# Performance work log

Measured on AMD Instinct MI355X. Metric: run time of the kernel, lower is better.

The kernel has to match this reference:

```python
import jax, jax.numpy as jnp
import numpy as np

T, K = 2048, 6          # tokens, activated experts per token
DIM = 2048              # model dim
INTER = 1408            # moe intermediate dim
E = 16                  # routed experts (group_size, shared not fused)


def setup_inputs() -> dict:
    key = jax.random.key(0)
    k1, k2, k3, k4, k5, k6 = jax.random.split(key, 6)
    x = jax.random.normal(k1, (T, DIM), dtype=jnp.float32)
    weights = jax.random.uniform(k2, (T, K), dtype=jnp.float32)
    indices = jax.random.randint(k3, (T, K), 0, E, dtype=jnp.int64)
    s = 1.0 / np.sqrt(DIM)
    Wg = jax.random.normal(k4, (E, INTER, DIM), dtype=jnp.float32) * s
    Wu = jax.random.normal(k5, (E, INTER, DIM), dtype=jnp.float32) * s
    Wd = jax.random.normal(k6, (E, DIM, INTER), dtype=jnp.float32) * (1.0 / np.sqrt(INTER))
    return {"x": x, "weights": weights, "indices": indices,
            "Wg": Wg, "Wu": Wu, "Wd": Wd}


def reference(x, weights, indices, Wg, Wu, Wd):
    # per-token combine weight for each expert: [T, E]
    # gate_w[t, e] = sum_k weights[t, k] * (indices[t, k] == e)
    one_hot = jax.nn.one_hot(indices, E, dtype=x.dtype)        # [T, K, E]
    gate_w = jnp.einsum('tk,tke->te', weights, one_hot)        # [T, E]

    # SwiGLU expert FFN, dense over experts, combine folded pre-down-proj
    g = jnp.einsum('td,eid->tei', x, Wg)                       # [T, E, INTER]
    u = jnp.einsum('td,eid->tei', x, Wu)                       # [T, E, INTER]
    act = jax.nn.silu(g) * u                                   # [T, E, INTER]
    # y[t] = sum_e gate_w[t,e] * (act[t,e] @ Wd[e].T)
    y = jnp.einsum('tei,edi->td', act * gate_w[:, :, None], Wd)  # [T, DIM]
    return y
```

## Files before the change

kernel.cpp:

```cpp
#include <hip/hip_runtime.h>
#include <hip/hip_bf16.h>
#include <cstdint>

#define TT     2048
#define KSEL   6
#define DMODEL 2048
#define DINTER 1408
#define NE     16
#define PMAX   (TT * KSEL)

typedef short bf16x8 __attribute__((ext_vector_type(8)));
typedef float f32x4 __attribute__((ext_vector_type(4)));
typedef unsigned short u16;
typedef u16 u16x8 __attribute__((ext_vector_type(8)));

__device__ __forceinline__ u16 f2bf(float f) {
  union { float f; unsigned u; } v; v.f = f;
  return (u16)((v.u + 0x7FFFu + ((v.u >> 16) & 1u)) >> 16);
}

__device__ __forceinline__ void gl2lds16(const void* g, void* l) {
  __builtin_amdgcn_global_load_lds((const __attribute__((address_space(1))) void*)g,
                                   (__attribute__((address_space(3))) void*)l,
                                   16, 0, 0);
}

__global__ void k_gate(const float* __restrict__ w, const int* __restrict__ idx,
                       float* __restrict__ gate_w, int* __restrict__ counts) {
  int g = blockIdx.x * 256 + threadIdx.x;
  int t = g >> 4, e = g & 15;
  const int* ip = idx + t * KSEL;
  const float* wp = w + t * KSEL;
  float s = 0.f;
#pragma unroll
  for (int k = 0; k < KSEL; ++k) s += (ip[k] == e) ? wp[k] : 0.f;
  gate_w[g] = s;
  if (s != 0.f) atomicAdd(counts + e, 1);
}

__global__ void k_scan(const int* __restrict__ counts, int* __restrict__ offs) {
  if (threadIdx.x == 0 && blockIdx.x == 0) {
    int r = 0;
#pragma unroll
    for (int e = 0; e < NE; ++e) { offs[e] = r; r += counts[e]; }
    offs[NE] = r;
  }
}

__global__ void k_fill(const float* __restrict__ gate_w, const int* __restrict__ offs,
                       int* __restrict__ cursor, int* __restrict__ slot_tok,
                       float* __restrict__ slot_gate) {
  int g = blockIdx.x * 256 + threadIdx.x;
  int t = g >> 4, e = g & 15;
  float s = gate_w[g];
  if (s != 0.f) {
    int p = atomicAdd(cursor + e, 1);
    int sl = offs[e] + p;
    slot_tok[sl] = t;
    slot_gate[sl] = s;
  }
}

#define XV8   (TT * DMODEL / 8)
#define WV8   (NE * DINTER * DMODEL / 8)
__global__ void k_castall(const float* __restrict__ x,  u16* __restrict__ xb,
                          const float* __restrict__ wg, u16* __restrict__ wgb,
                          const float* __restrict__ wu, u16* __restrict__ wub,
                          const float* __restrict__ wd, u16* __restrict__ wdb) {
  const int total = XV8 + 3 * WV8;
  int stride = gridDim.x * 256;
  for (int i = blockIdx.x * 256 + threadIdx.x; i < total; i += stride) {
    const float* src; u16* dst; int j;
    if (i < XV8)                { src = x;  dst = xb;  j = i; }
    else if (i < XV8 + WV8)     { src = wg; dst = wgb; j = i - XV8; }
    else if (i < XV8 + 2 * WV8) { src = wu; dst = wub; j = i - XV8 - WV8; }
    else                        { src = wd; dst = wdb; j = i - XV8 - 2 * WV8; }
    const float4* p = (const float4*)src + (size_t)j * 2;
    float4 v0 = p[0], v1 = p[1];
    u16x8 o;
    o[0] = f2bf(v0.x); o[1] = f2bf(v0.y); o[2] = f2bf(v0.z); o[3] = f2bf(v0.w);
    o[4] = f2bf(v1.x); o[5] = f2bf(v1.y); o[6] = f2bf(v1.z); o[7] = f2bf(v1.w);
    *(u16x8*)(dst + (size_t)j * 8) = o;
  }
}


__global__ __launch_bounds__(256, 2) void k_gemm1(
    const u16* __restrict__ xb, const u16* __restrict__ wgb, const u16* __restrict__ wub,
    const int* __restrict__ slot_tok, const float* __restrict__ slot_gate,
    const int* __restrict__ offs, const int* __restrict__ counts,
    u16* __restrict__ act) {
  int b = blockIdx.x;
  int w = (b & 7) * 352 + (b >> 3);
  int mt = w & 15, rest = w >> 4;
  int it = rest % 11, e = rest / 11;

  int mcount = counts[e];
  if (mt * 128 >= mcount) return;
  int mrem = mcount - mt * 128; if (mrem > 128) mrem = 128;
  int slotBase = offs[e] + mt * 128;
  int iBase = it * 128;

  __shared__ u16 sA[128 * 64];
  __shared__ u16 sG[128 * 64];
  __shared__ u16 sU[128 * 64];
  __shared__ int tokLds[128];
  __shared__ float gateLds[128];

  int tid = threadIdx.x;
  if (tid < 128) {
    int rl = tid < mrem ? tid : 0;
    tokLds[tid] = slot_tok[slotBase + rl];
    gateLds[tid] = (tid < mrem) ? slot_gate[slotBase + rl] : 0.f;
  }
  __syncthreads();

  int wv = tid >> 6, lane = tid & 63;
  const u16 *aSrc[4], *gSrc[4], *uSrc[4];
  u16 *aDst[4], *gDst[4], *uDst[4];
  const u16* gBase = wgb + ((size_t)e * DINTER + iBase) * DMODEL;
  const u16* uBase = wub + ((size_t)e * DINTER + iBase) * DMODEL;
  int r8 = lane >> 3;
  int colOff = (((lane & 7) ^ r8)) * 8;
#pragma unroll
  for (int i2 = 0; i2 < 4; ++i2) {
    int chunk = wv * 4 + i2;
    int row = chunk * 8 + r8;
    aSrc[i2] = xb + (size_t)tokLds[row] * DMODEL + colOff;
    gSrc[i2] = gBase + (size_t)row * DMODEL + colOff;
    uSrc[i2] = uBase + (size_t)row * DMODEL + colOff;
    aDst[i2] = sA + chunk * 512;
    gDst[i2] = sG + chunk * 512;
    uDst[i2] = sU + chunk * 512;
  }

  f32x4 accg[4][4] = {};
  f32x4 accu[4][4] = {};
  int fr = lane & 15, fq = lane >> 4;
  int wr = (wv >> 1) * 64, wc = (wv & 1) * 64;

  for (int kb = 0; kb < DMODEL / 64; ++kb) {
    int kOff = kb * 64;
    __syncthreads();
#pragma unroll
    for (int i2 = 0; i2 < 4; ++i2) {
      gl2lds16(aSrc[i2] + kOff, aDst[i2]);
      gl2lds16(gSrc[i2] + kOff, gDst[i2]);
      gl2lds16(uSrc[i2] + kOff, uDst[i2]);
    }
    __syncthreads();
#pragma unroll
    for (int kf = 0; kf < 2; ++kf) {
      bf16x8 af[4], bg[4], bu[4];
#pragma unroll
      for (int mf = 0; mf < 4; ++mf) {
        int row = wr + mf * 16 + fr;
        int cu = ((kf * 4 + fq) ^ (row & 7)) * 8;
        af[mf] = *(const bf16x8*)&sA[row * 64 + cu];
      }
#pragma unroll
      for (int nf = 0; nf < 4; ++nf) {
        int row = wc + nf * 16 + fr;
        int cu = ((kf * 4 + fq) ^ (row & 7)) * 8;
        bg[nf] = *(const bf16x8*)&sG[row * 64 + cu];
        bu[nf] = *(const bf16x8*)&sU[row * 64 + cu];
      }
#pragma unroll
      for (int mf = 0; mf < 4; ++mf)
#pragma unroll
        for (int nf = 0; nf < 4; ++nf) {
          accg[mf][nf] = __builtin_amdgcn_mfma_f32_16x16x32_bf16(af[mf], bg[nf], accg[mf][nf], 0, 0, 0);
          accu[mf][nf] = __builtin_amdgcn_mfma_f32_16x16x32_bf16(af[mf], bu[nf], accu[mf][nf], 0, 0, 0);
        }
    }
  }
#pragma unroll
  for (int mf = 0; mf < 4; ++mf)
#pragma unroll
    for (int nf = 0; nf < 4; ++nf)
#pragma unroll
      for (int r = 0; r < 4; ++r) {
        int row = wr + mf * 16 + fq * 4 + r;
        if (row < mrem) {
          float g = accg[mf][nf][r], u = accu[mf][nf][r];
          float a = g / (1.f + __expf(-g)) * u * gateLds[row];
          act[(size_t)(slotBase + row) * DINTER + iBase + wc + nf * 16 + fr] = f2bf(a);
        }
      }
}

__global__ __launch_bounds__(256, 4) void k_gemm2(
    const u16* __restrict__ act, const u16* __restrict__ wdb,
    const int* __restrict__ slot_tok, const int* __restrict__ offs,
    const int* __restrict__ counts, float* __restrict__ y) {
  int b = blockIdx.x;
  int w = (b & 7) * 512 + (b >> 3);
  int mt = w & 15, rest = w >> 4;
  int dt = rest & 15, e = rest >> 4;

  int mcount = counts[e];
  if (mt * 128 >= mcount) return;
  int mrem = mcount - mt * 128; if (mrem > 128) mrem = 128;
  int slotBase = offs[e] + mt * 128;
  int dBase = dt * 128;

  __shared__ u16 sA[128 * 64];
  __shared__ u16 sB[128 * 64];
  __shared__ int tokLds[128];

  int tid = threadIdx.x;
  if (tid < 128) tokLds[tid] = slot_tok[slotBase + (tid < mrem ? tid : 0)];
  __syncthreads();

  int wv = tid >> 6, lane = tid & 63;
  const u16 *aSrc[4], *bSrc[4];
  u16 *aDst[4], *bDst[4];
  const u16* bBase = wdb + ((size_t)e * DMODEL + dBase) * DINTER;
  int r8 = lane >> 3;
  int colOff = (((lane & 7) ^ r8)) * 8;
#pragma unroll
  for (int i2 = 0; i2 < 4; ++i2) {
    int chunk = wv * 4 + i2;
    int row = chunk * 8 + r8;
    aSrc[i2] = act + (size_t)(slotBase + row) * DINTER + colOff;
    bSrc[i2] = bBase + (size_t)row * DINTER + colOff;
    aDst[i2] = sA + chunk * 512;
    bDst[i2] = sB + chunk * 512;
  }

  f32x4 acc[4][4] = {};
  int fr = lane & 15, fq = lane >> 4;
  int wr = (wv >> 1) * 64, wc = (wv & 1) * 64;

  for (int kb = 0; kb < DINTER / 64; ++kb) {
    int kOff = kb * 64;
    __syncthreads();
#pragma unroll
    for (int i2 = 0; i2 < 4; ++i2) {
      gl2lds16(aSrc[i2] + kOff, aDst[i2]);
      gl2lds16(bSrc[i2] + kOff, bDst[i2]);
    }
    __syncthreads();
#pragma unroll
    for (int kf = 0; kf < 2; ++kf) {
      bf16x8 af[4], bb[4];
#pragma unroll
      for (int mf = 0; mf < 4; ++mf) {
        int row = wr + mf * 16 + fr;
        int cu = ((kf * 4 + fq) ^ (row & 7)) * 8;
        af[mf] = *(const bf16x8*)&sA[row * 64 + cu];
      }
#pragma unroll
      for (int nf = 0; nf < 4; ++nf) {
        int row = wc + nf * 16 + fr;
        int cu = ((kf * 4 + fq) ^ (row & 7)) * 8;
        bb[nf] = *(const bf16x8*)&sB[row * 64 + cu];
      }
#pragma unroll
      for (int mf = 0; mf < 4; ++mf)
#pragma unroll
        for (int nf = 0; nf < 4; ++nf)
          acc[mf][nf] = __builtin_amdgcn_mfma_f32_16x16x32_bf16(af[mf], bb[nf], acc[mf][nf], 0, 0, 0);
    }
  }
#pragma unroll
  for (int mf = 0; mf < 4; ++mf)
#pragma unroll
    for (int nf = 0; nf < 4; ++nf)
#pragma unroll
      for (int r = 0; r < 4; ++r) {
        int row = wr + mf * 16 + fq * 4 + r;
        if (row < mrem) {
          int t = tokLds[row];
          atomicAdd(y + (size_t)t * DMODEL + dBase + wc + nf * 16 + fr, acc[mf][nf][r]);
        }
      }
}

extern "C" void kernel_launch(void* const* d_in, const int* in_sizes, int n_in,
                              void* d_out, int out_size, void* d_ws, size_t ws_size,
                              hipStream_t stream) {
  const float* x       = (const float*)d_in[0];
  const float* weights = (const float*)d_in[1];
  const int*   indices = (const int*)d_in[2];
  const float* Wg      = (const float*)d_in[3];
  const float* Wu      = (const float*)d_in[4];
  const float* Wd      = (const float*)d_in[5];
  float* y = (float*)d_out;

  const size_t WELEM = (size_t)NE * DINTER * DMODEL;

  char* ws = (char*)d_ws;
  size_t o = 0;
  float* gate_w = (float*)(ws + o); o += (size_t)TT * NE * 4;
  size_t ctrlOff = o;
  int* counts = (int*)(ws + o);
  int* offs   = (int*)(ws + o + 64);
  int* cursor = (int*)(ws + o + 192);
  o += 256;
  int*   slot_tok  = (int*)(ws + o);   o += (size_t)PMAX * 4;
  float* slot_gate = (float*)(ws + o); o += (size_t)PMAX * 4;
  u16* xb  = (u16*)(ws + o); o += (size_t)TT * DMODEL * 2;
  u16* act = (u16*)(ws + o); o += (size_t)(PMAX + 128) * DINTER * 2;
  u16* wgb = (u16*)(ws + o); o += WELEM * 2;
  u16* wub = (u16*)(ws + o); o += WELEM * 2;
  u16* wdb = (u16*)(ws + o); o += WELEM * 2;
  (void)ws_size; (void)in_sizes; (void)n_in;

  hipMemsetAsync(d_out, 0, (size_t)out_size * 4, stream);
  hipMemsetAsync(ws + ctrlOff, 0, 256, stream);

  k_gate<<<TT * NE / 256, 256, 0, stream>>>(weights, indices, gate_w, counts);
  k_scan<<<1, 64, 0, stream>>>(counts, offs);
  k_fill<<<TT * NE / 256, 256, 0, stream>>>(gate_w, offs, cursor, slot_tok, slot_gate);
  k_castall<<<2048, 256, 0, stream>>>(x, xb, Wg, wgb, Wu, wub, Wd, wdb);
  k_gemm1<<<2816, 256, 0, stream>>>(xb, wgb, wub, slot_tok, slot_gate, offs, counts, act);
  k_gemm2<<<4096, 256, 0, stream>>>(act, wdb, slot_tok, offs, counts, y);
}
```

Baseline: 592.1 us.

## Rebuild gate/up GEMM as 256x128 tile with a four-stage async LDS pipeline

The gate/up projection kernel now uses 512 threads per block and a 256-row token tile, so each loaded weight tile is reused across twice as many tokens. The K loop becomes 32-wide steps over four LDS buffers filled by asynchronous global-to-LDS loads. Loads are issued interleaved with the gate and up MFMA phases, with explicit vmcnt waits, barriers and s_setprio around the MFMA bursts. The aim is to hide global load latency behind compute and cut weight traffic. In exchange it uses about 130 KB of LDS, so only one block fits per CU despite the launch bounds, and the hand-tuned barrier scheme is fragile.

```diff
diff --git a/kernel.cpp b/kernel.cpp
--- a/kernel.cpp
+++ b/kernel.cpp
@@ -24,6 +24,11 @@
                                    (__attribute__((address_space(3))) void*)l,
                                    16, 0, 0);
 }
+
+#define BOUNDARY(N) do { \
+  asm volatile("s_waitcnt vmcnt(" #N ")" ::: "memory"); \
+  __builtin_amdgcn_s_barrier(); \
+} while (0)
 
 __global__ void k_gate(const float* __restrict__ w, const int* __restrict__ idx,
                        float* __restrict__ gate_w, int* __restrict__ counts) {
@@ -84,31 +89,33 @@
   }
 }
 
-
-__global__ __launch_bounds__(256, 2) void k_gemm1(
+#define AB 8192
+#define GB 4096
+
+__global__ __launch_bounds__(512, 2) void k_gemm1(
     const u16* __restrict__ xb, const u16* __restrict__ wgb, const u16* __restrict__ wub,
     const int* __restrict__ slot_tok, const float* __restrict__ slot_gate,
     const int* __restrict__ offs, const int* __restrict__ counts,
     u16* __restrict__ act) {
   int b = blockIdx.x;
-  int w = (b & 7) * 352 + (b >> 3);
-  int mt = w & 15, rest = w >> 4;
+  int w = (b & 7) * 176 + (b >> 3);
+  int mt = w & 7, rest = w >> 3;
   int it = rest % 11, e = rest / 11;
 
   int mcount = counts[e];
-  if (mt * 128 >= mcount) return;
-  int mrem = mcount - mt * 128; if (mrem > 128) mrem = 128;
-  int slotBase = offs[e] + mt * 128;
+  if (mt * 256 >= mcount) return;
+  int mrem = mcount - mt * 256; if (mrem > 256) mrem = 256;
+  int slotBase = offs[e] + mt * 256;
   int iBase = it * 128;
 
-  __shared__ u16 sA[128 * 64];
-  __shared__ u16 sG[128 * 64];
-  __shared__ u16 sU[128 * 64];
-  __shared__ int tokLds[128];
-  __shared__ float gateLds[128];
+  __shared__ u16 sA[4 * AB];
+  __shared__ u16 sG[4 * GB];
+  __shared__ u16 sU[4 * GB];
+  __shared__ int tokLds[256];
+  __shared__ float gateLds[256];
 
   int tid = threadIdx.x;
-  if (tid < 128) {
+  if (tid < 256) {
     int rl = tid < mrem ? tid : 0;
     tokLds[tid] = slot_tok[slotBase + rl];
     gateLds[tid] = (tid < mrem) ? slot_gate[slotBase + rl] : 0.f;
@@ -116,64 +123,95 @@
   __syncthreads();
 
   int wv = tid >> 6, lane = tid & 63;
-  const u16 *aSrc[4], *gSrc[4], *uSrc[4];
-  u16 *aDst[4], *gDst[4], *uDst[4];
-  const u16* gBase = wgb + ((size_t)e * DINTER + iBase) * DMODEL;
-  const u16* uBase = wub + ((size_t)e * DINTER + iBase) * DMODEL;
-  int r8 = lane >> 3;
-  int colOff = (((lane & 7) ^ r8)) * 8;
-#pragma unroll
-  for (int i2 = 0; i2 < 4; ++i2) {
-    int chunk = wv * 4 + i2;
-    int row = chunk * 8 + r8;
-    aSrc[i2] = xb + (size_t)tokLds[row] * DMODEL + colOff;
-    gSrc[i2] = gBase + (size_t)row * DMODEL + colOff;
-    uSrc[i2] = uBase + (size_t)row * DMODEL + colOff;
-    aDst[i2] = sA + chunk * 512;
-    gDst[i2] = sG + chunk * 512;
-    uDst[i2] = sU + chunk * 512;
+  int rIC = lane >> 2;
+  int uSw = ((lane & 3) ^ ((rIC >> 1) & 3)) * 8;
+  const u16 *aSrc0, *aSrc1, *gSrc, *uSrc;
+  int aOff0, aOff1, gOff;
+  {
+    const u16* gBase = wgb + ((size_t)e * DINTER + iBase) * DMODEL;
+    const u16* uBase = wub + ((size_t)e * DINTER + iBase) * DMODEL;
+    int c0 = wv * 2, c1 = wv * 2 + 1;
+    aSrc0 = xb + (size_t)tokLds[c0 * 16 + rIC] * DMODEL + uSw;
+    aSrc1 = xb + (size_t)tokLds[c1 * 16 + rIC] * DMODEL + uSw;
+    aOff0 = c0 * 512; aOff1 = c1 * 512;
+    gSrc = gBase + (size_t)(wv * 16 + rIC) * DMODEL + uSw;
+    uSrc = uBase + (size_t)(wv * 16 + rIC) * DMODEL + uSw;
+    gOff = wv * 512;
   }
 
   f32x4 accg[4][4] = {};
   f32x4 accu[4][4] = {};
   int fr = lane & 15, fq = lane >> 4;
   int wr = (wv >> 1) * 64, wc = (wv & 1) * 64;
-
-  for (int kb = 0; kb < DMODEL / 64; ++kb) {
-    int kOff = kb * 64;
-    __syncthreads();
-#pragma unroll
-    for (int i2 = 0; i2 < 4; ++i2) {
-      gl2lds16(aSrc[i2] + kOff, aDst[i2]);
-      gl2lds16(gSrc[i2] + kOff, gDst[i2]);
-      gl2lds16(uSrc[i2] + kOff, uDst[i2]);
+  int aRd[4], bRd[4];
+#pragma unroll
+  for (int mf = 0; mf < 4; ++mf) {
+    int row = wr + mf * 16 + fr;
+    aRd[mf] = row * 32 + ((fq ^ ((row >> 1) & 3)) << 3);
+  }
+#pragma unroll
+  for (int nf = 0; nf < 4; ++nf) {
+    int row = wc + nf * 16 + fr;
+    bRd[nf] = row * 32 + ((fq ^ ((row >> 1) & 3)) << 3);
+  }
+
+  auto STAGE4 = [&](int bs, int kS) {
+    gl2lds16(aSrc0 + kS, &sA[bs * AB + aOff0]);
+    gl2lds16(aSrc1 + kS, &sA[bs * AB + aOff1]);
+    gl2lds16(gSrc + kS, &sG[bs * GB + gOff]);
+    gl2lds16(uSrc + kS, &sU[bs * GB + gOff]);
+  };
+
+  auto TILE = [&](int bf, int bs, int kS, bool doStage) {
+    if (doStage) {
+      gl2lds16(aSrc0 + kS, &sA[bs * AB + aOff0]);
+      gl2lds16(aSrc1 + kS, &sA[bs * AB + aOff1]);
     }
-    __syncthreads();
-#pragma unroll
-    for (int kf = 0; kf < 2; ++kf) {
-      bf16x8 af[4], bg[4], bu[4];
-#pragma unroll
-      for (int mf = 0; mf < 4; ++mf) {
-        int row = wr + mf * 16 + fr;
-        int cu = ((kf * 4 + fq) ^ (row & 7)) * 8;
-        af[mf] = *(const bf16x8*)&sA[row * 64 + cu];
-      }
-#pragma unroll
-      for (int nf = 0; nf < 4; ++nf) {
-        int row = wc + nf * 16 + fr;
-        int cu = ((kf * 4 + fq) ^ (row & 7)) * 8;
-        bg[nf] = *(const bf16x8*)&sG[row * 64 + cu];
-        bu[nf] = *(const bf16x8*)&sU[row * 64 + cu];
-      }
-#pragma unroll
-      for (int mf = 0; mf < 4; ++mf)
-#pragma unroll
-        for (int nf = 0; nf < 4; ++nf) {
-          accg[mf][nf] = __builtin_amdgcn_mfma_f32_16x16x32_bf16(af[mf], bg[nf], accg[mf][nf], 0, 0, 0);
-          accu[mf][nf] = __builtin_amdgcn_mfma_f32_16x16x32_bf16(af[mf], bu[nf], accu[mf][nf], 0, 0, 0);
-        }
+    bf16x8 af[4], bg[4], bu[4];
+#pragma unroll
+    for (int mf = 0; mf < 4; ++mf) af[mf] = *(const bf16x8*)&sA[bf * AB + aRd[mf]];
+#pragma unroll
+    for (int nf = 0; nf < 4; ++nf) bg[nf] = *(const bf16x8*)&sG[bf * GB + bRd[nf]];
+    __builtin_amdgcn_s_barrier();
+    __builtin_amdgcn_s_setprio(1);
+#pragma unroll
+    for (int mf = 0; mf < 4; ++mf)
+#pragma unroll
+      for (int nf = 0; nf < 4; ++nf)
+        accg[mf][nf] = __builtin_amdgcn_mfma_f32_16x16x32_bf16(af[mf], bg[nf], accg[mf][nf], 0, 0, 0);
+    __builtin_amdgcn_s_setprio(0);
+    __builtin_amdgcn_s_barrier();
+    if (doStage) {
+      gl2lds16(gSrc + kS, &sG[bs * GB + gOff]);
+      gl2lds16(uSrc + kS, &sU[bs * GB + gOff]);
     }
-  }
+#pragma unroll
+    for (int nf = 0; nf < 4; ++nf) bu[nf] = *(const bf16x8*)&sU[bf * GB + bRd[nf]];
+    __builtin_amdgcn_s_barrier();
+    __builtin_amdgcn_s_setprio(1);
+#pragma unroll
+    for (int mf = 0; mf < 4; ++mf)
+#pragma unroll
+      for (int nf = 0; nf < 4; ++nf)
+        accu[mf][nf] = __builtin_amdgcn_mfma_f32_16x16x32_bf16(af[mf], bu[nf], accu[mf][nf], 0, 0, 0);
+    __builtin_amdgcn_s_setprio(0);
+  };
+
+  STAGE4(0, 0);
+  STAGE4(1, 32);
+  BOUNDARY(4);
+#pragma unroll 1
+  for (int t4 = 0; t4 < 60; t4 += 4) {
+    TILE(0, 2, (t4 + 2) * 32, true);  BOUNDARY(4);
+    TILE(1, 3, (t4 + 3) * 32, true);  BOUNDARY(4);
+    TILE(2, 0, (t4 + 4) * 32, true);  BOUNDARY(4);
+    TILE(3, 1, (t4 + 5) * 32, true);  BOUNDARY(4);
+  }
+  TILE(0, 2, 62 * 32, true);   BOUNDARY(4);
+  TILE(1, 3, 63 * 32, true);   BOUNDARY(4);
+  TILE(2, 0, 0, false);        BOUNDARY(0);
+  TILE(3, 0, 0, false);
+
 #pragma unroll
   for (int mf = 0; mf < 4; ++mf)
 #pragma unroll
@@ -301,7 +339,7 @@
   int*   slot_tok  = (int*)(ws + o);   o += (size_t)PMAX * 4;
   float* slot_gate = (float*)(ws + o); o += (size_t)PMAX * 4;
   u16* xb  = (u16*)(ws + o); o += (size_t)TT * DMODEL * 2;
-  u16* act = (u16*)(ws + o); o += (size_t)(PMAX + 128) * DINTER * 2;
+  u16* act = (u16*)(ws + o); o += (size_t)(PMAX + 256) * DINTER * 2;
   u16* wgb = (u16*)(ws + o); o += WELEM * 2;
   u16* wub = (u16*)(ws + o); o += WELEM * 2;
   u16* wdb = (u16*)(ws + o); o += WELEM * 2;
@@ -314,6 +352,6 @@
   k_scan<<<1, 64, 0, stream>>>(counts, offs);
   k_fill<<<TT * NE / 256, 256, 0, stream>>>(gate_w, offs, cursor, slot_tok, slot_gate);
   k_castall<<<2048, 256, 0, stream>>>(x, xb, Wg, wgb, Wu, wub, Wd, wdb);
-  k_gemm1<<<2816, 256, 0, stream>>>(xb, wgb, wub, slot_tok, slot_gate, offs, counts, act);
+  k_gemm1<<<1408, 512, 0, stream>>>(xb, wgb, wub, slot_tok, slot_gate, offs, counts, act);
   k_gemm2<<<4096, 256, 0, stream>>>(act, wdb, slot_tok, offs, counts, y);
 }
```

New measurement: 615.6 us. 1.04x slower.

## Fuse fp32-to-bf16 weight conversion into GEMM tile loads with register prefetch

Applied to the files above, without the earlier changes.

Removes the separate pass that casts all expert weights to bf16. Each GEMM now reads fp32 weight tiles straight into registers, converts them and writes them swizzled into LDS, while the next tile is prefetched into registers. This saves writing and re-reading the bf16 weight copies, but every block that shares a weight tile re-reads fp32 data (twice the bytes) and repeats the conversion. It also raises register pressure (gemm2 occupancy hint lowered to 3) and drops the XCD-aware block remapping.

```diff
diff --git a/kernel.cpp b/kernel.cpp
--- a/kernel.cpp
+++ b/kernel.cpp
@@ -19,11 +19,19 @@
   return (u16)((v.u + 0x7FFFu + ((v.u >> 16) & 1u)) >> 16);
 }
 
+__device__ __forceinline__ u16 f2bfh(float f) {
+  __hip_bfloat16 h = __float2bfloat16(f);
+  u16 r; __builtin_memcpy(&r, &h, 2); return r;
+}
+
 __device__ __forceinline__ void gl2lds16(const void* g, void* l) {
   __builtin_amdgcn_global_load_lds((const __attribute__((address_space(1))) void*)g,
                                    (__attribute__((address_space(3))) void*)l,
                                    16, 0, 0);
 }
+
+#define BAR_RAW() asm volatile("s_barrier" ::: "memory")
+#define DRAIN() asm volatile("s_waitcnt vmcnt(0) lgkmcnt(0)" ::: "memory")
 
 __global__ void k_gate(const float* __restrict__ w, const int* __restrict__ idx,
                        float* __restrict__ gate_w, int* __restrict__ counts) {
@@ -61,38 +69,23 @@
   }
 }
 
-#define XV8   (TT * DMODEL / 8)
-#define WV8   (NE * DINTER * DMODEL / 8)
-__global__ void k_castall(const float* __restrict__ x,  u16* __restrict__ xb,
-                          const float* __restrict__ wg, u16* __restrict__ wgb,
-                          const float* __restrict__ wu, u16* __restrict__ wub,
-                          const float* __restrict__ wd, u16* __restrict__ wdb) {
-  const int total = XV8 + 3 * WV8;
-  int stride = gridDim.x * 256;
-  for (int i = blockIdx.x * 256 + threadIdx.x; i < total; i += stride) {
-    const float* src; u16* dst; int j;
-    if (i < XV8)                { src = x;  dst = xb;  j = i; }
-    else if (i < XV8 + WV8)     { src = wg; dst = wgb; j = i - XV8; }
-    else if (i < XV8 + 2 * WV8) { src = wu; dst = wub; j = i - XV8 - WV8; }
-    else                        { src = wd; dst = wdb; j = i - XV8 - 2 * WV8; }
-    const float4* p = (const float4*)src + (size_t)j * 2;
-    float4 v0 = p[0], v1 = p[1];
-    u16x8 o;
-    o[0] = f2bf(v0.x); o[1] = f2bf(v0.y); o[2] = f2bf(v0.z); o[3] = f2bf(v0.w);
-    o[4] = f2bf(v1.x); o[5] = f2bf(v1.y); o[6] = f2bf(v1.z); o[7] = f2bf(v1.w);
-    *(u16x8*)(dst + (size_t)j * 8) = o;
-  }
-}
-
+__global__ void k_castx(const float* __restrict__ x, u16* __restrict__ xb) {
+  int i = blockIdx.x * 256 + threadIdx.x;
+  const float4* p = (const float4*)x + (size_t)i * 2;
+  float4 v0 = p[0], v1 = p[1];
+  u16x8 o;
+  o[0] = f2bf(v0.x); o[1] = f2bf(v0.y); o[2] = f2bf(v0.z); o[3] = f2bf(v0.w);
+  o[4] = f2bf(v1.x); o[5] = f2bf(v1.y); o[6] = f2bf(v1.z); o[7] = f2bf(v1.w);
+  *(u16x8*)(xb + (size_t)i * 8) = o;
+}
 
 __global__ __launch_bounds__(256, 2) void k_gemm1(
-    const u16* __restrict__ xb, const u16* __restrict__ wgb, const u16* __restrict__ wub,
+    const u16* __restrict__ xb, const float* __restrict__ Wg, const float* __restrict__ Wu,
     const int* __restrict__ slot_tok, const float* __restrict__ slot_gate,
     const int* __restrict__ offs, const int* __restrict__ counts,
     u16* __restrict__ act) {
   int b = blockIdx.x;
-  int w = (b & 7) * 352 + (b >> 3);
-  int mt = w & 15, rest = w >> 4;
+  int mt = b & 15, rest = b >> 4;
   int it = rest % 11, e = rest / 11;
 
   int mcount = counts[e];
@@ -116,39 +109,59 @@
   __syncthreads();
 
   int wv = tid >> 6, lane = tid & 63;
-  const u16 *aSrc[4], *gSrc[4], *uSrc[4];
-  u16 *aDst[4], *gDst[4], *uDst[4];
-  const u16* gBase = wgb + ((size_t)e * DINTER + iBase) * DMODEL;
-  const u16* uBase = wub + ((size_t)e * DINTER + iBase) * DMODEL;
+  const u16* aSrc[4]; u16* aDst[4];
   int r8 = lane >> 3;
-  int colOff = (((lane & 7) ^ r8)) * 8;
+  int colOff = ((lane & 7) ^ r8) * 8;
 #pragma unroll
   for (int i2 = 0; i2 < 4; ++i2) {
     int chunk = wv * 4 + i2;
     int row = chunk * 8 + r8;
     aSrc[i2] = xb + (size_t)tokLds[row] * DMODEL + colOff;
-    gSrc[i2] = gBase + (size_t)row * DMODEL + colOff;
-    uSrc[i2] = uBase + (size_t)row * DMODEL + colOff;
     aDst[i2] = sA + chunk * 512;
-    gDst[i2] = sG + chunk * 512;
-    uDst[i2] = sU + chunk * 512;
-  }
+  }
+
+  int srow = tid >> 1, sc0 = (tid & 1) * 32;
+  const float* gS = Wg + ((size_t)e * DINTER + iBase + srow) * DMODEL + sc0;
+  const float* uS = Wu + ((size_t)e * DINTER + iBase + srow) * DMODEL + sc0;
+  int wrBase = srow * 64;
+  int u4 = (tid & 1) * 4;
+
+  f32x4 vg[8], vu[8];
+  auto LOADB = [&](int kk) {
+#pragma unroll
+    for (int j = 0; j < 8; ++j) {
+      vg[j] = *(const f32x4*)(gS + kk * 64 + j * 4);
+      vu[j] = *(const f32x4*)(uS + kk * 64 + j * 4);
+    }
+  };
 
   f32x4 accg[4][4] = {};
   f32x4 accu[4][4] = {};
   int fr = lane & 15, fq = lane >> 4;
   int wr = (wv >> 1) * 64, wc = (wv & 1) * 64;
 
+  LOADB(0);
+
+#pragma unroll 1
   for (int kb = 0; kb < DMODEL / 64; ++kb) {
-    int kOff = kb * 64;
-    __syncthreads();
-#pragma unroll
-    for (int i2 = 0; i2 < 4; ++i2) {
-      gl2lds16(aSrc[i2] + kOff, aDst[i2]);
-      gl2lds16(gSrc[i2] + kOff, gDst[i2]);
-      gl2lds16(uSrc[i2] + kOff, uDst[i2]);
-    }
-    __syncthreads();
+    BAR_RAW();
+#pragma unroll
+    for (int i2 = 0; i2 < 4; ++i2) gl2lds16(aSrc[i2] + kb * 64, aDst[i2]);
+#pragma unroll
+    for (int w = 0; w < 4; ++w) {
+      union { u16 h[8]; bf16x8 v; } og, ou;
+#pragma unroll
+      for (int q = 0; q < 8; ++q) {
+        og.h[q] = f2bfh(vg[w * 2 + (q >> 2)][q & 3]);
+        ou.h[q] = f2bfh(vu[w * 2 + (q >> 2)][q & 3]);
+      }
+      int du = (((u4 + w) ^ (srow & 7)) << 3);
+      *(bf16x8*)&sG[wrBase + du] = og.v;
+      *(bf16x8*)&sU[wrBase + du] = ou.v;
+    }
+    DRAIN();
+    LOADB((kb + 1) & 31);
+    BAR_RAW();
 #pragma unroll
     for (int kf = 0; kf < 2; ++kf) {
       bf16x8 af[4], bg[4], bu[4];
@@ -189,13 +202,12 @@
       }
 }
 
-__global__ __launch_bounds__(256, 4) void k_gemm2(
-    const u16* __restrict__ act, const u16* __restrict__ wdb,
+__global__ __launch_bounds__(256, 3) void k_gemm2(
+    const u16* __restrict__ act, const float* __restrict__ Wd,
     const int* __restrict__ slot_tok, const int* __restrict__ offs,
     const int* __restrict__ counts, float* __restrict__ y) {
   int b = blockIdx.x;
-  int w = (b & 7) * 512 + (b >> 3);
-  int mt = w & 15, rest = w >> 4;
+  int mt = b & 15, rest = b >> 4;
   int dt = rest & 15, e = rest >> 4;
 
   int mcount = counts[e];
@@ -213,34 +225,51 @@
   __syncthreads();
 
   int wv = tid >> 6, lane = tid & 63;
-  const u16 *aSrc[4], *bSrc[4];
-  u16 *aDst[4], *bDst[4];
-  const u16* bBase = wdb + ((size_t)e * DMODEL + dBase) * DINTER;
+  const u16* aSrc[4]; u16* aDst[4];
   int r8 = lane >> 3;
-  int colOff = (((lane & 7) ^ r8)) * 8;
+  int colOff = ((lane & 7) ^ r8) * 8;
 #pragma unroll
   for (int i2 = 0; i2 < 4; ++i2) {
     int chunk = wv * 4 + i2;
     int row = chunk * 8 + r8;
     aSrc[i2] = act + (size_t)(slotBase + row) * DINTER + colOff;
-    bSrc[i2] = bBase + (size_t)row * DINTER + colOff;
     aDst[i2] = sA + chunk * 512;
-    bDst[i2] = sB + chunk * 512;
-  }
+  }
+
+  int srow = tid >> 1, sc0 = (tid & 1) * 32;
+  const float* bS = Wd + ((size_t)e * DMODEL + dBase + srow) * DINTER + sc0;
+  int wrBase = srow * 64;
+  int u4 = (tid & 1) * 4;
+
+  f32x4 vb[8];
+  auto LOADB = [&](int kk) {
+#pragma unroll
+    for (int j = 0; j < 8; ++j) vb[j] = *(const f32x4*)(bS + kk * 64 + j * 4);
+  };
 
   f32x4 acc[4][4] = {};
   int fr = lane & 15, fq = lane >> 4;
   int wr = (wv >> 1) * 64, wc = (wv & 1) * 64;
 
-  for (int kb = 0; kb < DINTER / 64; ++kb) {
-    int kOff = kb * 64;
-    __syncthreads();
-#pragma unroll
-    for (int i2 = 0; i2 < 4; ++i2) {
-      gl2lds16(aSrc[i2] + kOff, aDst[i2]);
-      gl2lds16(bSrc[i2] + kOff, bDst[i2]);
-    }
-    __syncthreads();
+  const int NT = DINTER / 64;
+  LOADB(0);
+
+#pragma unroll 1
+  for (int kb = 0; kb < NT; ++kb) {
+    BAR_RAW();
+#pragma unroll
+    for (int i2 = 0; i2 < 4; ++i2) gl2lds16(aSrc[i2] + kb * 64, aDst[i2]);
+#pragma unroll
+    for (int w = 0; w < 4; ++w) {
+      union { u16 h[8]; bf16x8 v; } ob;
+#pragma unroll
+      for (int q = 0; q < 8; ++q) ob.h[q] = f2bfh(vb[w * 2 + (q >> 2)][q & 3]);
+      int du = (((u4 + w) ^ (srow & 7)) << 3);
+      *(bf16x8*)&sB[wrBase + du] = ob.v;
+    }
+    DRAIN();
+    LOADB((kb + 1 == NT) ? 0 : kb + 1);
+    BAR_RAW();
 #pragma unroll
     for (int kf = 0; kf < 2; ++kf) {
       bf16x8 af[4], bb[4];
@@ -287,8 +316,6 @@
   const float* Wu      = (const float*)d_in[4];
   const float* Wd      = (const float*)d_in[5];
   float* y = (float*)d_out;
-
-  const size_t WELEM = (size_t)NE * DINTER * DMODEL;
 
   char* ws = (char*)d_ws;
   size_t o = 0;
@@ -301,10 +328,7 @@
   int*   slot_tok  = (int*)(ws + o);   o += (size_t)PMAX * 4;
   float* slot_gate = (float*)(ws + o); o += (size_t)PMAX * 4;
   u16* xb  = (u16*)(ws + o); o += (size_t)TT * DMODEL * 2;
-  u16* act = (u16*)(ws + o); o += (size_t)(PMAX + 128) * DINTER * 2;
-  u16* wgb = (u16*)(ws + o); o += WELEM * 2;
-  u16* wub = (u16*)(ws + o); o += WELEM * 2;
-  u16* wdb = (u16*)(ws + o); o += WELEM * 2;
+  u16* act = (u16*)(ws + o); o += (size_t)(PMAX + 256) * DINTER * 2;
   (void)ws_size; (void)in_sizes; (void)n_in;
 
   hipMemsetAsync(d_out, 0, (size_t)out_size * 4, stream);
@@ -313,7 +337,7 @@
   k_gate<<<TT * NE / 256, 256, 0, stream>>>(weights, indices, gate_w, counts);
   k_scan<<<1, 64, 0, stream>>>(counts, offs);
   k_fill<<<TT * NE / 256, 256, 0, stream>>>(gate_w, offs, cursor, slot_tok, slot_gate);
-  k_castall<<<2048, 256, 0, stream>>>(x, xb, Wg, wgb, Wu, wub, Wd, wdb);
-  k_gemm1<<<2816, 256, 0, stream>>>(xb, wgb, wub, slot_tok, slot_gate, offs, counts, act);
-  k_gemm2<<<4096, 256, 0, stream>>>(act, wdb, slot_tok, offs, counts, y);
-}
+  k_castx<<<(TT * DMODEL / 8) / 256, 256, 0, stream>>>(x, xb);
+  k_gemm1<<<2816, 256, 0, stream>>>(xb, Wg, Wu, slot_tok, slot_gate, offs, counts, act);
+  k_gemm2<<<4096, 256, 0, stream>>>(act, Wd, slot_tok, offs, counts, y);
+}
```

Result: slower. 1.657 ms (+179.8%).

## Overlap Wd cast inside gemm1 grid and widen gemm2 to two N tiles

Applied to the files above, without the earlier changes.

The Wd fp32-to-bf16 cast moves out of the standalone cast kernel and into extra blocks interleaved with the gemm1 grid, one in every five. The aim is to hide that memory-bound work behind the gate/up GEMM. gemm2 now computes two 128-wide output column tiles per block, sharing the A (activation) tile and halving the grid. This cuts A reloads and block count, but raises register pressure, so launch bounds drop from 4 to 3.

```diff
diff --git a/kernel.cpp b/kernel.cpp
--- a/kernel.cpp
+++ b/kernel.cpp
@@ -63,18 +63,16 @@
 
 #define XV8   (TT * DMODEL / 8)
 #define WV8   (NE * DINTER * DMODEL / 8)
-__global__ void k_castall(const float* __restrict__ x,  u16* __restrict__ xb,
-                          const float* __restrict__ wg, u16* __restrict__ wgb,
-                          const float* __restrict__ wu, u16* __restrict__ wub,
-                          const float* __restrict__ wd, u16* __restrict__ wdb) {
-  const int total = XV8 + 3 * WV8;
+__global__ void k_cast3(const float* __restrict__ x,  u16* __restrict__ xb,
+                        const float* __restrict__ wg, u16* __restrict__ wgb,
+                        const float* __restrict__ wu, u16* __restrict__ wub) {
+  const int total = XV8 + 2 * WV8;
   int stride = gridDim.x * 256;
   for (int i = blockIdx.x * 256 + threadIdx.x; i < total; i += stride) {
     const float* src; u16* dst; int j;
-    if (i < XV8)                { src = x;  dst = xb;  j = i; }
-    else if (i < XV8 + WV8)     { src = wg; dst = wgb; j = i - XV8; }
-    else if (i < XV8 + 2 * WV8) { src = wu; dst = wub; j = i - XV8 - WV8; }
-    else                        { src = wd; dst = wdb; j = i - XV8 - 2 * WV8; }
+    if (i < XV8)            { src = x;  dst = xb;  j = i; }
+    else if (i < XV8 + WV8) { src = wg; dst = wgb; j = i - XV8; }
+    else                    { src = wu; dst = wub; j = i - XV8 - WV8; }
     const float4* p = (const float4*)src + (size_t)j * 2;
     float4 v0 = p[0], v1 = p[1];
     u16x8 o;
@@ -84,14 +82,30 @@
   }
 }
 
-
 __global__ __launch_bounds__(256, 2) void k_gemm1(
     const u16* __restrict__ xb, const u16* __restrict__ wgb, const u16* __restrict__ wub,
+    const float* __restrict__ Wd, u16* __restrict__ wdb,
     const int* __restrict__ slot_tok, const float* __restrict__ slot_gate,
     const int* __restrict__ offs, const int* __restrict__ counts,
     u16* __restrict__ act) {
-  int b = blockIdx.x;
-  int w = (b & 7) * 352 + (b >> 3);
+  int bq = blockIdx.x >> 3, br = blockIdx.x & 7;
+  if (bq % 5 == 4) {
+    int c = (bq / 5) * 8 + br;
+    int base = c * 8192;
+#pragma unroll 4
+    for (int it = 0; it < 32; ++it) {
+      int j = base + it * 256 + threadIdx.x;
+      const float4* p = (const float4*)Wd + (size_t)j * 2;
+      float4 v0 = p[0], v1 = p[1];
+      u16x8 o;
+      o[0] = f2bf(v0.x); o[1] = f2bf(v0.y); o[2] = f2bf(v0.z); o[3] = f2bf(v0.w);
+      o[4] = f2bf(v1.x); o[5] = f2bf(v1.y); o[6] = f2bf(v1.z); o[7] = f2bf(v1.w);
+      *(u16x8*)(wdb + (size_t)j * 8) = o;
+    }
+    return;
+  }
+  int g = ((bq / 5) * 4 + (bq % 5)) * 8 + br;
+  int w = (g & 7) * 352 + (g >> 3);
   int mt = w & 15, rest = w >> 4;
   int it = rest % 11, e = rest / 11;
 
@@ -121,7 +135,7 @@
   const u16* gBase = wgb + ((size_t)e * DINTER + iBase) * DMODEL;
   const u16* uBase = wub + ((size_t)e * DINTER + iBase) * DMODEL;
   int r8 = lane >> 3;
-  int colOff = (((lane & 7) ^ r8)) * 8;
+  int colOff = ((lane & 7) ^ r8) * 8;
 #pragma unroll
   for (int i2 = 0; i2 < 4; ++i2) {
     int chunk = wv * 4 + i2;
@@ -182,30 +196,31 @@
       for (int r = 0; r < 4; ++r) {
         int row = wr + mf * 16 + fq * 4 + r;
         if (row < mrem) {
-          float g = accg[mf][nf][r], u = accu[mf][nf][r];
-          float a = g / (1.f + __expf(-g)) * u * gateLds[row];
+          float gv = accg[mf][nf][r], uv = accu[mf][nf][r];
+          float a = gv / (1.f + __expf(-gv)) * uv * gateLds[row];
           act[(size_t)(slotBase + row) * DINTER + iBase + wc + nf * 16 + fr] = f2bf(a);
         }
       }
 }
 
-__global__ __launch_bounds__(256, 4) void k_gemm2(
+__global__ __launch_bounds__(256, 3) void k_gemm2(
     const u16* __restrict__ act, const u16* __restrict__ wdb,
     const int* __restrict__ slot_tok, const int* __restrict__ offs,
     const int* __restrict__ counts, float* __restrict__ y) {
   int b = blockIdx.x;
-  int w = (b & 7) * 512 + (b >> 3);
+  int w = (b & 7) * 256 + (b >> 3);
   int mt = w & 15, rest = w >> 4;
-  int dt = rest & 15, e = rest >> 4;
+  int dtp = rest & 7, e = rest >> 3;
 
   int mcount = counts[e];
   if (mt * 128 >= mcount) return;
   int mrem = mcount - mt * 128; if (mrem > 128) mrem = 128;
   int slotBase = offs[e] + mt * 128;
-  int dBase = dt * 128;
+  int dBase0 = dtp * 256, dBase1 = dtp * 256 + 128;
 
   __shared__ u16 sA[128 * 64];
-  __shared__ u16 sB[128 * 64];
+  __shared__ u16 sB0[128 * 64];
+  __shared__ u16 sB1[128 * 64];
   __shared__ int tokLds[128];
 
   int tid = threadIdx.x;
@@ -213,22 +228,26 @@
   __syncthreads();
 
   int wv = tid >> 6, lane = tid & 63;
-  const u16 *aSrc[4], *bSrc[4];
-  u16 *aDst[4], *bDst[4];
-  const u16* bBase = wdb + ((size_t)e * DMODEL + dBase) * DINTER;
+  const u16 *aSrc[4], *b0Src[4], *b1Src[4];
+  u16 *aDst[4], *b0Dst[4], *b1Dst[4];
+  const u16* b0Base = wdb + ((size_t)e * DMODEL + dBase0) * DINTER;
+  const u16* b1Base = wdb + ((size_t)e * DMODEL + dBase1) * DINTER;
   int r8 = lane >> 3;
-  int colOff = (((lane & 7) ^ r8)) * 8;
+  int colOff = ((lane & 7) ^ r8) * 8;
 #pragma unroll
   for (int i2 = 0; i2 < 4; ++i2) {
     int chunk = wv * 4 + i2;
     int row = chunk * 8 + r8;
-    aSrc[i2] = act + (size_t)(slotBase + row) * DINTER + colOff;
-    bSrc[i2] = bBase + (size_t)row * DINTER + colOff;
-    aDst[i2] = sA + chunk * 512;
-    bDst[i2] = sB + chunk * 512;
-  }
-
-  f32x4 acc[4][4] = {};
+    aSrc[i2]  = act + (size_t)(slotBase + row) * DINTER + colOff;
+    b0Src[i2] = b0Base + (size_t)row * DINTER + colOff;
+    b1Src[i2] = b1Base + (size_t)row * DINTER + colOff;
+    aDst[i2]  = sA  + chunk * 512;
+    b0Dst[i2] = sB0 + chunk * 512;
+    b1Dst[i2] = sB1 + chunk * 512;
+  }
+
+  f32x4 acc0[4][4] = {};
+  f32x4 acc1[4][4] = {};
   int fr = lane & 15, fq = lane >> 4;
   int wr = (wv >> 1) * 64, wc = (wv & 1) * 64;
 
@@ -238,12 +257,13 @@
 #pragma unroll
     for (int i2 = 0; i2 < 4; ++i2) {
       gl2lds16(aSrc[i2] + kOff, aDst[i2]);
-      gl2lds16(bSrc[i2] + kOff, bDst[i2]);
+      gl2lds16(b0Src[i2] + kOff, b0Dst[i2]);
+      gl2lds16(b1Src[i2] + kOff, b1Dst[i2]);
     }
     __syncthreads();
 #pragma unroll
     for (int kf = 0; kf < 2; ++kf) {
-      bf16x8 af[4], bb[4];
+      bf16x8 af[4], bb0[4], bb1[4];
 #pragma unroll
       for (int mf = 0; mf < 4; ++mf) {
         int row = wr + mf * 16 + fr;
@@ -254,13 +274,16 @@
       for (int nf = 0; nf < 4; ++nf) {
         int row = wc + nf * 16 + fr;
         int cu = ((kf * 4 + fq) ^ (row & 7)) * 8;
-        bb[nf] = *(const bf16x8*)&sB[row * 64 + cu];
+        bb0[nf] = *(const bf16x8*)&sB0[row * 64 + cu];
+        bb1[nf] = *(const bf16x8*)&sB1[row * 64 + cu];
       }
 #pragma unroll
       for (int mf = 0; mf < 4; ++mf)
 #pragma unroll
-        for (int nf = 0; nf < 4; ++nf)
-          acc[mf][nf] = __builtin_amdgcn_mfma_f32_16x16x32_bf16(af[mf], bb[nf], acc[mf][nf], 0, 0, 0);
+        for (int nf = 0; nf < 4; ++nf) {
+          acc0[mf][nf] = __builtin_amdgcn_mfma_f32_16x16x32_bf16(af[mf], bb0[nf], acc0[mf][nf], 0, 0, 0);
+          acc1[mf][nf] = __builtin_amdgcn_mfma_f32_16x16x32_bf16(af[mf], bb1[nf], acc1[mf][nf], 0, 0, 0);
+        }
     }
   }
 #pragma unroll
@@ -272,7 +295,8 @@
         int row = wr + mf * 16 + fq * 4 + r;
         if (row < mrem) {
           int t = tokLds[row];
-          atomicAdd(y + (size_t)t * DMODEL + dBase + wc + nf * 16 + fr, acc[mf][nf][r]);
+          atomicAdd(y + (size_t)t * DMODEL + dBase0 + wc + nf * 16 + fr, acc0[mf][nf][r]);
+          atomicAdd(y + (size_t)t * DMODEL + dBase1 + wc + nf * 16 + fr, acc1[mf][nf][r]);
         }
       }
 }
@@ -301,7 +325,7 @@
   int*   slot_tok  = (int*)(ws + o);   o += (size_t)PMAX * 4;
   float* slot_gate = (float*)(ws + o); o += (size_t)PMAX * 4;
   u16* xb  = (u16*)(ws + o); o += (size_t)TT * DMODEL * 2;
-  u16* act = (u16*)(ws + o); o += (size_t)(PMAX + 128) * DINTER * 2;
+  u16* act = (u16*)(ws + o); o += (size_t)(PMAX + 256) * DINTER * 2;
   u16* wgb = (u16*)(ws + o); o += WELEM * 2;
   u16* wub = (u16*)(ws + o); o += WELEM * 2;
   u16* wdb = (u16*)(ws + o); o += WELEM * 2;
@@ -313,7 +337,8 @@
   k_gate<<<TT * NE / 256, 256, 0, stream>>>(weights, indices, gate_w, counts);
   k_scan<<<1, 64, 0, stream>>>(counts, offs);
   k_fill<<<TT * NE / 256, 256, 0, stream>>>(gate_w, offs, cursor, slot_tok, slot_gate);
-  k_castall<<<2048, 256, 0, stream>>>(x, xb, Wg, wgb, Wu, wub, Wd, wdb);
-  k_gemm1<<<2816, 256, 0, stream>>>(xb, wgb, wub, slot_tok, slot_gate, offs, counts, act);
-  k_gemm2<<<4096, 256, 0, stream>>>(act, wdb, slot_tok, offs, counts, y);
-}
+  k_cast3<<<2048, 256, 0, stream>>>(x, xb, Wg, wgb, Wu, wub);
+  k_gemm1<<<3520, 256, 0, stream>>>(xb, wgb, wub, Wd, wdb, slot_tok, slot_gate,
+                                    offs, counts, act);
+  k_gemm2<<<2048, 256, 0, stream>>>(act, wdb, slot_tok, offs, counts, y);
+}
```

Result: slower. 724.4 us (+22.3%).
